# Performance work log

Measured on AMD Instinct MI355X. Metric: run time of the kernel, lower is better.

The kernel has to match this reference:

```python
import jax, jax.numpy as jnp
import numpy as np

B, S, H, L = 64, 512, 1024, 5  # batch, seq_len, BiLSTM feature dim (2*512), num fine P labels


def setup_inputs() -> dict:
    key = jax.random.key(0)
    ks = jax.random.split(key, 8)
    feats = jax.random.normal(ks[0], (B, S, H), dtype=jnp.float32)
    labels = jax.random.randint(ks[1], (B, S), 0, L)
    mask = jnp.ones((B, S), dtype=bool)  # CRF requires mask[:, 0] all on
    W_tag = jax.random.normal(ks[2], (H, L), dtype=jnp.float32) * 0.02
    b_tag = jnp.zeros((L,), dtype=jnp.float32)
    start_trans = jax.random.normal(ks[3], (L,), dtype=jnp.float32) * 0.1
    end_trans = jax.random.normal(ks[4], (L,), dtype=jnp.float32) * 0.1
    trans = jax.random.normal(ks[5], (L, L), dtype=jnp.float32) * 0.1
    weights = jax.random.uniform(ks[6], (L,), dtype=jnp.float32, minval=0.5, maxval=1.5)
    return dict(feats=feats, labels=labels, mask=mask, W_tag=W_tag, b_tag=b_tag,
                start_trans=start_trans, end_trans=end_trans, trans=trans, weights=weights)


def reference(feats, labels, mask, W_tag, b_tag, start_trans, end_trans, trans, weights):
    # hidden2tag + relu (as in the torch module: probablity = F.relu(self.hidden2tag(...)))
    emissions = jax.nn.relu(feats @ W_tag + b_tag)  # [B, S, L]
    maskf = mask.astype(emissions.dtype)            # [B, S]

    # ---- weighted CRF negative log-likelihood, reduction='token_mean' ----
    # numerator: gold-path score, per-token emission contributions scaled by class weights
    em_tag = jnp.take_along_axis(emissions, labels[..., None], axis=2)[..., 0]  # [B, S]
    numerator = (start_trans[labels[:, 0]]
                 + jnp.sum(weights[labels] * em_tag * maskf, axis=1)
                 + jnp.sum(trans[labels[:, :-1], labels[:, 1:]] * maskf[:, 1:], axis=1)
                 + end_trans[labels[:, -1]])  # [B]

    # partition function via forward algorithm (scan over time)
    emis_t = emissions[:, 1:].swapaxes(0, 1)  # [S-1, B, L]
    mask_t = mask[:, 1:].T                    # [S-1, B]

    def fwd_step(alpha, x):
        e, m = x  # [B, L], [B]
        new = jax.nn.logsumexp(alpha[:, :, None] + trans[None, :, :], axis=1) + e
        return jnp.where(m[:, None], new, alpha), None

    alpha0 = start_trans[None, :] + emissions[:, 0]  # [B, L]
    alpha, _ = jax.lax.scan(fwd_step, alpha0, (emis_t, mask_t))
    log_z = jax.nn.logsumexp(alpha + end_trans[None, :], axis=1)  # [B]

    loss = -jnp.sum(numerator - log_z) / maskf.sum()

    # ---- Viterbi decode ----
    def vit_step(v, x):
        e, m = x
        scores = v[:, :, None] + trans[None, :, :]  # [B, L_prev, L_cur]
        best = jnp.max(scores, axis=1) + e
        idx = jnp.argmax(scores, axis=1)            # backpointers [B, L]
        return jnp.where(m[:, None], best, v), idx

    v, hist = jax.lax.scan(vit_step, start_trans[None, :] + emissions[:, 0], (emis_t, mask_t))
    last = jnp.argmax(v + end_trans[None, :], axis=1)  # [B] tag at position S-1
    b_idx = jnp.arange(labels.shape[0])

    def back_step(tag, bp):
        prev = bp[b_idx, tag]
        return prev, tag  # emit tag at position t+1

    first, path_rest = jax.lax.scan(back_step, last, hist, reverse=True)  # [B], [S-1, B]
    paths = jnp.concatenate([first[None, :], path_rest], axis=0).T  # [B, S]

    return loss, paths
```

## Files before the change

### kernel.cpp

```cpp
#include <hip/hip_runtime.h>

namespace {

constexpr int kB = 64, kS = 512, kH = 1024, kL = 5;
constexpr int kRows = kB * kS;
constexpr float kNegInf = -1e30f;

__global__ __launch_bounds__(256) void emis_kernel(
    const float* __restrict__ feats, const float* __restrict__ W,
    const float* __restrict__ b_tag, float* __restrict__ emis,
    float* __restrict__ out_loss, int nwaves) {
  if (blockIdx.x == 0 && threadIdx.x == 0) out_loss[0] = 0.0f;

  const int lane = threadIdx.x & 63;
  const int wave = blockIdx.x * (blockDim.x >> 6) + (threadIdx.x >> 6);

  float wreg[4][20];
#pragma unroll
  for (int k0 = 0; k0 < 4; ++k0) {
    const float4* wp =
        reinterpret_cast<const float4*>(W + (k0 * 256 + lane * 4) * kL);
#pragma unroll
    for (int q = 0; q < 5; ++q) {
      float4 w = wp[q];
      wreg[k0][q * 4 + 0] = w.x;
      wreg[k0][q * 4 + 1] = w.y;
      wreg[k0][q * 4 + 2] = w.z;
      wreg[k0][q * 4 + 3] = w.w;
    }
  }

  for (int row = wave; row < kRows; row += nwaves) {
    const float4* f4 = reinterpret_cast<const float4*>(feats + (size_t)row * kH);
    float acc[kL] = {0.f, 0.f, 0.f, 0.f, 0.f};
#pragma unroll
    for (int k0 = 0; k0 < 4; ++k0) {
      float4 f = f4[(k0 << 6) + lane];
      const float* wr = wreg[k0];
#pragma unroll
      for (int l = 0; l < kL; ++l) {
        acc[l] = fmaf(f.x, wr[l], acc[l]);
        acc[l] = fmaf(f.y, wr[5 + l], acc[l]);
        acc[l] = fmaf(f.z, wr[10 + l], acc[l]);
        acc[l] = fmaf(f.w, wr[15 + l], acc[l]);
      }
    }
#pragma unroll
    for (int off = 32; off >= 1; off >>= 1)
#pragma unroll
      for (int l = 0; l < kL; ++l) acc[l] += __shfl_xor(acc[l], off, 64);
    if (lane < kL)
      emis[(size_t)row * kL + lane] = fmaxf(acc[lane] + b_tag[lane], 0.0f);
  }
}

__global__ __launch_bounds__(1024) void scan_kernel(
    const float* __restrict__ emis, const int* __restrict__ labels,
    const float* __restrict__ start_trans, const float* __restrict__ end_trans,
    const float* __restrict__ trans, const float* __restrict__ weights,
    float* __restrict__ out_loss, float* __restrict__ out_paths) {
  const int b = blockIdx.x;
  const int tid = threadIdx.x;
  const int lane = tid & 63;
  const int wv = tid >> 6;

  __shared__ float e_lds[kS * kL];
  __shared__ unsigned char bp_lds[(kS - 1) * kL];
  __shared__ unsigned short f_a[kS], f_b[kS];
  __shared__ float M_lds[8 * 25];
  __shared__ double num_sh;
  __shared__ int last_sh;

  {
    const float4* src = reinterpret_cast<const float4*>(emis + (size_t)b * kS * kL);
    float4* dst = reinterpret_cast<float4*>(e_lds);
    for (int i = tid; i < kS * kL / 4; i += 1024) dst[i] = src[i];
  }
  __syncthreads();

  const int j = (lane < kL) ? lane : 0;

  if (wv == 0) {
    const bool act = lane < kL;
    float tf[kL];
#pragma unroll
    for (int i = 0; i < kL; ++i) tf[i] = trans[i * kL + j];
    float vd = start_trans[j] + e_lds[j];
    float e_cur = e_lds[kL + j];
    for (int t = 1; t < kS; ++t) {
      float e_nxt = (t + 1 < kS) ? e_lds[(t + 1) * kL + j] : 0.0f;
      float v0 = __shfl(vd, 0, 64), v1 = __shfl(vd, 1, 64),
            v2 = __shfl(vd, 2, 64), v3 = __shfl(vd, 3, 64),
            v4 = __shfl(vd, 4, 64);
      float best = v0 + tf[0];
      int bi = 0;
      float bb;
      bb = v1 + tf[1]; if (bb > best) { best = bb; bi = 1; }
      bb = v2 + tf[2]; if (bb > best) { best = bb; bi = 2; }
      bb = v3 + tf[3]; if (bb > best) { best = bb; bi = 3; }
      bb = v4 + tf[4]; if (bb > best) { best = bb; bi = 4; }
      vd = best + e_cur;
      if (act) bp_lds[(t - 1) * kL + lane] = (unsigned char)bi;
      e_cur = e_nxt;
    }
    float vj[kL];
#pragma unroll
    for (int i = 0; i < kL; ++i) vj[i] = __shfl(vd, i, 64);
    if (lane == 0) {
      float best = vj[0] + end_trans[0];
      int last = 0;
      for (int i = 1; i < kL; ++i) {
        float cc = vj[i] + end_trans[i];
        if (cc > best) { best = cc; last = i; }
      }
      last_sh = last;
    }
  } else if (wv == 1) {
    double num = 0.0;
    for (int t = lane; t < kS; t += 64) {
      int lt = labels[b * kS + t];
      num += (double)weights[lt] * (double)e_lds[t * kL + lt];
      if (t > 0) {
        int lp = labels[b * kS + t - 1];
        num += (double)trans[lp * kL + lt];
      }
    }
#pragma unroll
    for (int off = 32; off >= 1; off >>= 1) num += __shfl_xor(num, off, 64);
    if (lane == 0) {
      int l0 = labels[b * kS];
      int lS = labels[b * kS + kS - 1];
      num_sh = num + (double)start_trans[l0] + (double)end_trans[lS];
    }
  } else if (wv < 10) {
    const int c = wv - 2;
    const int t0 = 1 + 64 * c;
    const int t1 = (t0 + 64 < kS) ? (t0 + 64) : kS;
    const int ci = (lane < 25) ? (lane / 5) : 0;
    const int cj = (lane < 25) ? (lane % 5) : 0;
    float tf[kL];
#pragma unroll
    for (int k = 0; k < kL; ++k) tf[k] = trans[k * kL + cj];
    float m = (lane < 25 && ci == cj) ? 0.0f : kNegInf;
    float e_cur = e_lds[t0 * kL + cj];
    for (int t = t0; t < t1; ++t) {
      float e_nxt = (t + 1 < t1) ? e_lds[(t + 1) * kL + cj] : 0.0f;
      float m0 = __shfl(m, ci * 5 + 0, 64), m1 = __shfl(m, ci * 5 + 1, 64),
            m2 = __shfl(m, ci * 5 + 2, 64), m3 = __shfl(m, ci * 5 + 3, 64),
            m4 = __shfl(m, ci * 5 + 4, 64);
      float c0 = m0 + tf[0], c1 = m1 + tf[1], c2 = m2 + tf[2],
            c3 = m3 + tf[3], c4 = m4 + tf[4];
      float mx = fmaxf(fmaxf(fmaxf(c0, c1), fmaxf(c2, c3)), c4);
      float s = __expf(c0 - mx) + __expf(c1 - mx) + __expf(c2 - mx) +
                __expf(c3 - mx) + __expf(c4 - mx);
      m = mx + __logf(s) + e_cur;
      e_cur = e_nxt;
    }
    if (lane < 25) M_lds[c * 25 + lane] = m;
  }
  __syncthreads();

  if (tid < kS - 1) {
    const int base = tid * kL;
    unsigned int w = 0;
#pragma unroll
    for (int q = 0; q < kL; ++q)
      w |= (unsigned int)bp_lds[base + q] << (3 * q);
    f_a[tid + 1] = (unsigned short)w;
  }
  __syncthreads();

  unsigned short* src = f_a;
  unsigned short* dst = f_b;
  for (int off = 1; off < kS; off <<= 1) {
    unsigned short v = 0;
    if (tid >= 1 && tid < kS) {
      v = src[tid];
      if (tid + off < kS) {
        unsigned int a = v, g = src[tid + off], r = 0;
#pragma unroll
        for (int x = 0; x < kL; ++x) {
          unsigned int bx = (g >> (3 * x)) & 7u;
          r |= ((a >> (3 * bx)) & 7u) << (3 * x);
        }
        v = (unsigned short)r;
      }
      dst[tid] = v;
    }
    __syncthreads();
    unsigned short* tmp = src; src = dst; dst = tmp;
  }

  const int last = last_sh;
  if (tid < kS - 1) {
    unsigned short g = src[tid + 1];
    out_paths[(size_t)b * kS + tid] = (float)((g >> (3 * last)) & 7u);
  } else if (tid == kS - 1) {
    out_paths[(size_t)b * kS + tid] = (float)last;
  }

  if (wv == 1) {
    float alpha = start_trans[j] + e_lds[j];
#pragma unroll 1
    for (int c = 0; c < 8; ++c) {
      float a0 = __shfl(alpha, 0, 64), a1 = __shfl(alpha, 1, 64),
            a2 = __shfl(alpha, 2, 64), a3 = __shfl(alpha, 3, 64),
            a4 = __shfl(alpha, 4, 64);
      float c0 = a0 + M_lds[c * 25 + 0 + j], c1 = a1 + M_lds[c * 25 + 5 + j],
            c2 = a2 + M_lds[c * 25 + 10 + j], c3 = a3 + M_lds[c * 25 + 15 + j],
            c4 = a4 + M_lds[c * 25 + 20 + j];
      float mx = fmaxf(fmaxf(fmaxf(c0, c1), fmaxf(c2, c3)), c4);
      float s = __expf(c0 - mx) + __expf(c1 - mx) + __expf(c2 - mx) +
                __expf(c3 - mx) + __expf(c4 - mx);
      alpha = mx + __logf(s);
    }
    float aj[kL];
#pragma unroll
    for (int i = 0; i < kL; ++i) aj[i] = __shfl(alpha, i, 64);
    if (lane == 0) {
      float c0 = aj[0] + end_trans[0], c1 = aj[1] + end_trans[1],
            c2 = aj[2] + end_trans[2], c3 = aj[3] + end_trans[3],
            c4 = aj[4] + end_trans[4];
      float mx = fmaxf(fmaxf(fmaxf(c0, c1), fmaxf(c2, c3)), c4);
      float logz =
          mx + __logf(__expf(c0 - mx) + __expf(c1 - mx) + __expf(c2 - mx) +
                      __expf(c3 - mx) + __expf(c4 - mx));
      double term = num_sh - (double)logz;
      atomicAdd(out_loss, (float)(-term / (double)(kB * kS)));
    }
  }
}

}

extern "C" void kernel_launch(void* const* d_in, const int* in_sizes, int n_in,
                              void* d_out, int out_size, void* d_ws,
                              size_t ws_size, hipStream_t stream) {
  const float* feats = (const float*)d_in[0];
  const int* labels = (const int*)d_in[1];
  const float* W_tag = (const float*)d_in[3];
  const float* b_tag = (const float*)d_in[4];
  const float* start_trans = (const float*)d_in[5];
  const float* end_trans = (const float*)d_in[6];
  const float* trans = (const float*)d_in[7];
  const float* weights = (const float*)d_in[8];

  float* emis = (float*)d_ws;
  float* out = (float*)d_out;

  const int blocks = 1024;
  const int nwaves = blocks * 4;
  emis_kernel<<<blocks, 256, 0, stream>>>(feats, W_tag, b_tag, emis, out,
                                          nwaves);
  scan_kernel<<<kB, 1024, 0, stream>>>(emis, labels, start_trans, end_trans,
                                       trans, weights, out, out + 1);
}
```

Baseline: 262.0 us.

## Move Viterbi argmax off serial chain and recompute backpointers in parallel

The serial Viterbi loop now keeps only the max-plus values: it stores each step's score vector to LDS and no longer computes argmax or writes backpointers. After the sync, each of 511 threads recomputes its step's backpointers from the stored scores. The loop also reads cross-lane values with readlane instead of shfl, prefetches emissions four steps ahead, unrolls by four, and reads trans from a cached LDS copy. This shortens the latency-bound recurrence at the cost of more LDS and a redundant parallel argmax pass.

```diff
diff --git a/kernel.cpp b/kernel.cpp
--- a/kernel.cpp
+++ b/kernel.cpp
@@ -5,6 +5,10 @@
 constexpr int kB = 64, kS = 512, kH = 1024, kL = 5;
 constexpr int kRows = kB * kS;
 constexpr float kNegInf = -1e30f;
+
+__device__ inline float rl(float x, int i) {
+  return __uint_as_float(__builtin_amdgcn_readlane(__float_as_uint(x), i));
+}
 
 __global__ __launch_bounds__(256) void emis_kernel(
     const float* __restrict__ feats, const float* __restrict__ W,
@@ -64,8 +68,9 @@
   const int lane = tid & 63;
   const int wv = tid >> 6;
 
-  __shared__ float e_lds[kS * kL];
-  __shared__ unsigned char bp_lds[(kS - 1) * kL];
+  __shared__ float e_lds[(kS + 4) * kL];
+  __shared__ float v_lds[kS * kL];
+  __shared__ float t_lds[25];
   __shared__ unsigned short f_a[kS], f_b[kS];
   __shared__ float M_lds[8 * 25];
   __shared__ double num_sh;
@@ -75,6 +80,8 @@
     const float4* src = reinterpret_cast<const float4*>(emis + (size_t)b * kS * kL);
     float4* dst = reinterpret_cast<float4*>(e_lds);
     for (int i = tid; i < kS * kL / 4; i += 1024) dst[i] = src[i];
+    if (tid < 4 * kL) e_lds[kS * kL + tid] = 0.0f;
+    if (tid < 25) t_lds[tid] = trans[tid];
   }
   __syncthreads();
 
@@ -84,35 +91,33 @@
     const bool act = lane < kL;
     float tf[kL];
 #pragma unroll
-    for (int i = 0; i < kL; ++i) tf[i] = trans[i * kL + j];
+    for (int i = 0; i < kL; ++i) tf[i] = t_lds[i * kL + j];
     float vd = start_trans[j] + e_lds[j];
-    float e_cur = e_lds[kL + j];
+    if (act) v_lds[lane] = vd;
+    float e0 = e_lds[1 * kL + j], e1 = e_lds[2 * kL + j],
+          e2 = e_lds[3 * kL + j], e3 = e_lds[4 * kL + j];
+#pragma unroll 4
     for (int t = 1; t < kS; ++t) {
-      float e_nxt = (t + 1 < kS) ? e_lds[(t + 1) * kL + j] : 0.0f;
-      float v0 = __shfl(vd, 0, 64), v1 = __shfl(vd, 1, 64),
-            v2 = __shfl(vd, 2, 64), v3 = __shfl(vd, 3, 64),
-            v4 = __shfl(vd, 4, 64);
-      float best = v0 + tf[0];
-      int bi = 0;
-      float bb;
-      bb = v1 + tf[1]; if (bb > best) { best = bb; bi = 1; }
-      bb = v2 + tf[2]; if (bb > best) { best = bb; bi = 2; }
-      bb = v3 + tf[3]; if (bb > best) { best = bb; bi = 3; }
-      bb = v4 + tf[4]; if (bb > best) { best = bb; bi = 4; }
-      vd = best + e_cur;
-      if (act) bp_lds[(t - 1) * kL + lane] = (unsigned char)bi;
-      e_cur = e_nxt;
-    }
-    float vj[kL];
-#pragma unroll
-    for (int i = 0; i < kL; ++i) vj[i] = __shfl(vd, i, 64);
+      float en = e_lds[(t + 4) * kL + j];
+      float s0 = rl(vd, 0), s1 = rl(vd, 1), s2 = rl(vd, 2), s3 = rl(vd, 3),
+            s4 = rl(vd, 4);
+      float c0 = s0 + tf[0], c1 = s1 + tf[1], c2 = s2 + tf[2],
+            c3 = s3 + tf[3], c4 = s4 + tf[4];
+      float m = fmaxf(fmaxf(fmaxf(c0, c1), fmaxf(c2, c3)), c4);
+      vd = m + e0;
+      if (act) v_lds[t * kL + lane] = vd;
+      e0 = e1; e1 = e2; e2 = e3; e3 = en;
+    }
+    float v0 = rl(vd, 0), v1 = rl(vd, 1), v2 = rl(vd, 2), v3 = rl(vd, 3),
+          v4 = rl(vd, 4);
     if (lane == 0) {
-      float best = vj[0] + end_trans[0];
+      float best = v0 + end_trans[0];
       int last = 0;
-      for (int i = 1; i < kL; ++i) {
-        float cc = vj[i] + end_trans[i];
-        if (cc > best) { best = cc; last = i; }
-      }
+      float cc;
+      cc = v1 + end_trans[1]; if (cc > best) { best = cc; last = 1; }
+      cc = v2 + end_trans[2]; if (cc > best) { best = cc; last = 2; }
+      cc = v3 + end_trans[3]; if (cc > best) { best = cc; last = 3; }
+      cc = v4 + end_trans[4]; if (cc > best) { best = cc; last = 4; }
       last_sh = last;
     }
   } else if (wv == 1) {
@@ -122,7 +127,7 @@
       num += (double)weights[lt] * (double)e_lds[t * kL + lt];
       if (t > 0) {
         int lp = labels[b * kS + t - 1];
-        num += (double)trans[lp * kL + lt];
+        num += (double)t_lds[lp * kL + lt];
       }
     }
 #pragma unroll
@@ -140,7 +145,7 @@
     const int cj = (lane < 25) ? (lane % 5) : 0;
     float tf[kL];
 #pragma unroll
-    for (int k = 0; k < kL; ++k) tf[k] = trans[k * kL + cj];
+    for (int k = 0; k < kL; ++k) tf[k] = t_lds[k * kL + cj];
     float m = (lane < 25 && ci == cj) ? 0.0f : kNegInf;
     float e_cur = e_lds[t0 * kL + cj];
     for (int t = t0; t < t1; ++t) {
@@ -161,11 +166,21 @@
   __syncthreads();
 
   if (tid < kS - 1) {
-    const int base = tid * kL;
+    float v0 = v_lds[tid * kL + 0], v1 = v_lds[tid * kL + 1],
+          v2 = v_lds[tid * kL + 2], v3 = v_lds[tid * kL + 3],
+          v4 = v_lds[tid * kL + 4];
     unsigned int w = 0;
 #pragma unroll
-    for (int q = 0; q < kL; ++q)
-      w |= (unsigned int)bp_lds[base + q] << (3 * q);
+    for (int q = 0; q < kL; ++q) {
+      float best = v0 + t_lds[0 * kL + q];
+      int bi = 0;
+      float bb;
+      bb = v1 + t_lds[1 * kL + q]; if (bb > best) { best = bb; bi = 1; }
+      bb = v2 + t_lds[2 * kL + q]; if (bb > best) { best = bb; bi = 2; }
+      bb = v3 + t_lds[3 * kL + q]; if (bb > best) { best = bb; bi = 3; }
+      bb = v4 + t_lds[4 * kL + q]; if (bb > best) { best = bb; bi = 4; }
+      w |= (unsigned int)bi << (3 * q);
+    }
     f_a[tid + 1] = (unsigned short)w;
   }
   __syncthreads();
@@ -173,9 +188,8 @@
   unsigned short* src = f_a;
   unsigned short* dst = f_b;
   for (int off = 1; off < kS; off <<= 1) {
-    unsigned short v = 0;
     if (tid >= 1 && tid < kS) {
-      v = src[tid];
+      unsigned short v = src[tid];
       if (tid + off < kS) {
         unsigned int a = v, g = src[tid + off], r = 0;
 #pragma unroll
```

Result: faster. 233.1 us (median of 2 runs) (-11.0%).
